# Kernel optimization log

Hardware: AMD Instinct MI355X
Metric: run time of the kernel (lower is better)

## Reference

```python
import jax, jax.numpy as jnp
import numpy as np

D_MODEL = 1024
H = 16
D_HEAD = D_MODEL // H


def setup_inputs() -> dict:
    key = jax.random.key(0)
    ks = jax.random.split(key, 9)
    B, S = 2, 2048
    x = jax.random.normal(ks[0], (B, S, D_MODEL), dtype=jnp.float32)
    s = 1.0 / np.sqrt(D_HEAD)
    # per-head Q/K/V linears, stacked: W[h, out, in], b[h, out] (torch Linear: y = x W^T + b)
    Wq = jax.random.normal(ks[1], (H, D_HEAD, D_HEAD), dtype=jnp.float32) * s
    bq = jax.random.normal(ks[2], (H, D_HEAD), dtype=jnp.float32) * 0.01
    Wk = jax.random.normal(ks[3], (H, D_HEAD, D_HEAD), dtype=jnp.float32) * s
    bk = jax.random.normal(ks[4], (H, D_HEAD), dtype=jnp.float32) * 0.01
    Wv = jax.random.normal(ks[5], (H, D_HEAD, D_HEAD), dtype=jnp.float32) * s
    bv = jax.random.normal(ks[6], (H, D_HEAD), dtype=jnp.float32) * 0.01
    Wo = jax.random.normal(ks[7], (D_MODEL, D_MODEL), dtype=jnp.float32) / np.sqrt(D_MODEL)
    bo = jax.random.normal(ks[8], (D_MODEL,), dtype=jnp.float32) * 0.01
    return {"x": x, "Wq": Wq, "bq": bq, "Wk": Wk, "bk": bk,
            "Wv": Wv, "bv": bv, "Wo": Wo, "bo": bo}


def reference(x, Wq, bq, Wk, bk, Wv, bv, Wo, bo):
    B, S, D = x.shape
    xh = x.reshape(B, S, H, D_HEAD)  # split along feature dim, head-major
    q = jnp.einsum('bshi,hoi->bsho', xh, Wq) + bq
    k = jnp.einsum('bshi,hoi->bsho', xh, Wk) + bk
    v = jnp.einsum('bshi,hoi->bsho', xh, Wv) + bv
    scale = 1.0 / jnp.sqrt(jnp.asarray(D_HEAD, dtype=x.dtype))  # source scales by sqrt(d_model//h)
    scores = jnp.einsum('bqhd,bkhd->bhqk', q, k) * scale
    causal = jnp.tril(jnp.ones((S, S), dtype=bool))
    scores = jnp.where(causal, scores, -jnp.inf)
    attn = jax.nn.softmax(scores, axis=-1)
    out = jnp.einsum('bhqk,bkhd->bqhd', attn, v).reshape(B, S, D)
    return out @ Wo.T + bo
```

## Files before the change

kernel.cpp:

```cpp
#include <hip/hip_runtime.h>
#include <cstddef>

#define Bc 2
#define Sc 2048
#define Dc 1024
#define Hc 16
#define QSC 0.18033688011112042f

typedef short short8 __attribute__((ext_vector_type(8)));
typedef float floatx4 __attribute__((ext_vector_type(4)));
typedef unsigned short ushort_t;

#if __has_builtin(__builtin_amdgcn_exp2f)
#define EXP2F(x) __builtin_amdgcn_exp2f(x)
#else
#define EXP2F(x) exp2f(x)
#endif

__device__ __forceinline__ unsigned pack2bf(float a, float b) {
    unsigned ua = __float_as_uint(a) + 0x8000u;
    unsigned ub = __float_as_uint(b) + 0x8000u;
    return __builtin_amdgcn_perm(ub, ua, 0x07060302u);
}
__device__ __forceinline__ ushort_t f2bf(float f) {
    return (ushort_t)((__float_as_uint(f) + 0x8000u) >> 16);
}

template<int N>
__device__ __forceinline__ float row_ror(float x) {
    return __int_as_float(__builtin_amdgcn_update_dpp(
        0, __float_as_int(x), 0x120 + N, 0xF, 0xF, false));
}
__device__ __forceinline__ float rsum16(float x) {
    x += row_ror<1>(x); x += row_ror<2>(x);
    x += row_ror<4>(x); x += row_ror<8>(x);
    return x;
}

__global__ __launch_bounds__(256) void wcvt_kernel(
    const float* __restrict__ Wo, const float* __restrict__ Wq,
    const float* __restrict__ Wk, const float* __restrict__ Wv,
    ushort_t* __restrict__ WoB, ushort_t* __restrict__ Wqkvb)
{
    int idx = (blockIdx.x * 256 + threadIdx.x) * 8;
    const float* src; ushort_t* dst;
    if (idx < 1048576) { src = Wo + idx; dst = WoB + idx; }
    else {
        int r = idx - 1048576;
        int w = r >> 16, off = r & 65535;
        src = (w == 0 ? Wq : (w == 1 ? Wk : Wv)) + off;
        dst = Wqkvb + r;
    }
    float4 a = *(const float4*)src;
    float4 c = *(const float4*)(src + 4);
    uint4 o;
    o.x = pack2bf(a.x, a.y); o.y = pack2bf(a.z, a.w);
    o.z = pack2bf(c.x, c.y); o.w = pack2bf(c.z, c.w);
    *(uint4*)dst = o;
}

__global__ __launch_bounds__(256) void qkv_kernel(
    const float* __restrict__ x, const ushort_t* __restrict__ Wqkvb,
    const float* __restrict__ bq, const float* __restrict__ bk, const float* __restrict__ bv,
    ushort_t* __restrict__ Qb, ushort_t* __restrict__ Kb, ushort_t* __restrict__ VT)
{
    const int blk = blockIdx.x;
    const int st = blk & 31, h = (blk >> 5) & 15, b = blk >> 9;
    const int bh = b * Hc + h, s0 = st * 64;
    const int tid = threadIdx.x, wid = tid >> 6, lane = tid & 63;
    const int lr = lane & 15, quad = lane >> 4;

    __shared__ ushort_t Xs[64 * 72];
    __shared__ ushort_t Wsh[3 * 64 * 72];

    {
        int row = tid >> 2, cg = tid & 3;
        const float* xp = x + ((size_t)(b * Sc + s0 + row)) * Dc + h * 64 + cg * 16;
        float4 v0 = *(const float4*)xp;
        float4 v1 = *(const float4*)(xp + 4);
        float4 v2 = *(const float4*)(xp + 8);
        float4 v3 = *(const float4*)(xp + 12);
        uint4 p0, p1;
        p0.x = pack2bf(v0.x, v0.y); p0.y = pack2bf(v0.z, v0.w);
        p0.z = pack2bf(v1.x, v1.y); p0.w = pack2bf(v1.z, v1.w);
        p1.x = pack2bf(v2.x, v2.y); p1.y = pack2bf(v2.z, v2.w);
        p1.z = pack2bf(v3.x, v3.y); p1.w = pack2bf(v3.z, v3.w);
        *(uint4*)(Xs + row * 72 + cg * 16) = p0;
        *(uint4*)(Xs + row * 72 + cg * 16 + 8) = p1;
    }
    {
        const ushort_t* Wg = Wqkvb + (size_t)h * 4096;
#pragma unroll
        for (int s = 0; s < 6; ++s) {
            int c = tid + s * 256;
            int w = c >> 9, rem = c & 511, row = rem >> 3, part = rem & 7;
            *(short8*)(Wsh + (w * 64 + row) * 72 + part * 8) =
                *(const short8*)(Wg + (size_t)w * 65536 + row * 64 + part * 8);
        }
    }
    __syncthreads();

    short8 af0 = *(const short8*)(Xs + (wid * 16 + lr) * 72 + quad * 8);
    short8 af1 = *(const short8*)(Xs + (wid * 16 + lr) * 72 + 32 + quad * 8);

    const float* bias3[3] = {bq + h * 64, bk + h * 64, bv + h * 64};
    const int row = tid >> 2, cg = tid & 3;

#pragma unroll
    for (int w = 0; w < 3; ++w) {
        ushort_t* Ot = Wsh + w * 64 * 72;
        short8 bf0[4], bf1[4];
#pragma unroll
        for (int n = 0; n < 4; ++n) {
            const ushort_t* wrow = Ot + (n * 16 + lr) * 72;
            bf0[n] = *(const short8*)(wrow + quad * 8);
            bf1[n] = *(const short8*)(wrow + 32 + quad * 8);
        }
        floatx4 acc[4];
#pragma unroll
        for (int n = 0; n < 4; ++n) {
            floatx4 z = {0.f, 0.f, 0.f, 0.f};
            acc[n] = __builtin_amdgcn_mfma_f32_16x16x32_bf16(af0, bf0[n], z, 0, 0, 0);
            acc[n] = __builtin_amdgcn_mfma_f32_16x16x32_bf16(af1, bf1[n], acc[n], 0, 0, 0);
        }
        __syncthreads();
        if (w < 2) {
#pragma unroll
            for (int n = 0; n < 4; ++n) {
                float bias = bias3[w][n * 16 + lr];
#pragma unroll
                for (int r = 0; r < 4; ++r) {
                    float val = acc[n][r] + bias;
                    if (w == 0) val *= QSC;
                    Ot[(wid * 16 + quad * 4 + r) * 72 + n * 16 + lr] = f2bf(val);
                }
            }
        } else {
#pragma unroll
            for (int n = 0; n < 4; ++n) {
                float bias = bias3[2][n * 16 + lr];
                uint2 pw;
                pw.x = pack2bf(acc[n][0] + bias, acc[n][1] + bias);
                pw.y = pack2bf(acc[n][2] + bias, acc[n][3] + bias);
                *(uint2*)(Ot + (n * 16 + lr) * 72 + wid * 16 + quad * 4) = pw;
            }
        }
        __syncthreads();
        const ushort_t* srcp = Ot + row * 72 + cg * 16;
        uint4 d0 = *(const uint4*)srcp;
        uint4 d1 = *(const uint4*)(srcp + 8);
        ushort_t* dst;
        if (w == 0)      dst = Qb + ((size_t)bh * Sc + s0 + row) * 64 + cg * 16;
        else if (w == 1) dst = Kb + ((size_t)bh * Sc + s0 + row) * 64 + cg * 16;
        else             dst = VT + ((size_t)bh * 64 + row) * Sc + s0 + cg * 16;
        *(uint4*)dst = d0;
        *(uint4*)(dst + 8) = d1;
    }
}

#define ST 72

__global__ __launch_bounds__(128) void attn_kernel(
    const ushort_t* __restrict__ Qg, const ushort_t* __restrict__ Kg,
    const ushort_t* __restrict__ VTg, ushort_t* __restrict__ Actx)
{
    const int blk = blockIdx.x;
    const int u = blk & 255;
    const int bh = u & 31;
    const int f = (u >> 5) & 7;
    const int tpair = (blk < 256) ? f : 15 - f;
    const int b = bh >> 4, h = bh & 15;
    const int qta = 31 - tpair, qtb = tpair;
    const int s0a = qta * 64, s0b = qtb * 64;
    const int tid = threadIdx.x, wid = tid >> 6, lane = tid & 63;
    const int lr = lane & 15, quad = lane >> 4;

    __shared__ ushort_t Ks[64 * ST];
    __shared__ ushort_t Vs[64 * ST];
    __shared__ ushort_t Ps[8 * 16 * ST];

    const ushort_t* Kbh = Kg + (size_t)bh * Sc * 64;
    const ushort_t* Vbh = VTg + (size_t)bh * 64 * Sc;

    short8 qa[2][2], qb[2][2];
#pragma unroll
    for (int g = 0; g < 2; ++g) {
        const ushort_t* QrA = Qg + ((size_t)bh * Sc + s0a + wid * 32 + g * 16 + lr) * 64;
        const ushort_t* QrB = Qg + ((size_t)bh * Sc + s0b + wid * 32 + g * 16 + lr) * 64;
        qa[g][0] = *(const short8*)(QrA + quad * 8);
        qa[g][1] = *(const short8*)(QrA + 32 + quad * 8);
        qb[g][0] = *(const short8*)(QrB + quad * 8);
        qb[g][1] = *(const short8*)(QrB + 32 + quad * 8);
    }

    floatx4 oA[2][4], oB[2][4];
    float lA[2][4], lB[2][4];
#pragma unroll
    for (int g = 0; g < 2; ++g)
#pragma unroll
        for (int n = 0; n < 4; ++n) { oA[g][n] = floatx4{0,0,0,0}; oB[g][n] = floatx4{0,0,0,0}; }
#pragma unroll
    for (int g = 0; g < 2; ++g)
#pragma unroll
        for (int r = 0; r < 4; ++r) { lA[g][r] = 0.f; lB[g][r] = 0.f; }

    const int sr = tid >> 3, sp = tid & 7;

    short8 kr[4], vr[4];
#pragma unroll
    for (int s = 0; s < 4; ++s) {
        kr[s] = *(const short8*)(Kbh + (size_t)(sr + s * 16) * 64 + sp * 8);
        vr[s] = *(const short8*)(Vbh + (size_t)(sr + s * 16) * Sc + sp * 8);
    }
#pragma unroll
    for (int s = 0; s < 4; ++s) {
        *(short8*)(Ks + (sr + s * 16) * ST + sp * 8) = kr[s];
        *(short8*)(Vs + (sr + s * 16) * ST + sp * 8) = vr[s];
    }
    __syncthreads();

    for (int kt = 0; kt <= qta; ++kt) {
        const bool hasB = (kt <= qtb);

        short8 kf[4][2];
#pragma unroll
        for (int kg = 0; kg < 4; ++kg) {
            const ushort_t* kp = Ks + (4 * lr + kg) * ST;
            kf[kg][0] = *(const short8*)(kp + quad * 8);
            kf[kg][1] = *(const short8*)(kp + 32 + quad * 8);
        }

        if (kt < qta) {
            const ushort_t* kn = Kbh + (size_t)(kt + 1) * 4096;
            const ushort_t* vn = Vbh + (kt + 1) * 64;
#pragma unroll
            for (int s = 0; s < 4; ++s) {
                kr[s] = *(const short8*)(kn + (size_t)(sr + s * 16) * 64 + sp * 8);
                vr[s] = *(const short8*)(vn + (size_t)(sr + s * 16) * Sc + sp * 8);
            }
        }

#pragma unroll
        for (int g = 0; g < 2; ++g) {
            floatx4 s4[4];
#pragma unroll
            for (int kg = 0; kg < 4; ++kg) {
                floatx4 z = {0.f, 0.f, 0.f, 0.f};
                floatx4 t0 = __builtin_amdgcn_mfma_f32_16x16x32_bf16(qa[g][0], kf[kg][0], z, 0, 0, 0);
                s4[kg] = __builtin_amdgcn_mfma_f32_16x16x32_bf16(qa[g][1], kf[kg][1], t0, 0, 0, 0);
            }
            if (kt == qta) {
#pragma unroll
                for (int kg = 0; kg < 4; ++kg) {
                    int key = 4 * lr + kg;
#pragma unroll
                    for (int r = 0; r < 4; ++r)
                        if (key > wid * 32 + g * 16 + quad * 4 + r) s4[kg][r] = -1e30f;
                }
            }
            ushort_t* Pg = Ps + ((wid * 2 + g) * 16) * ST;
#pragma unroll
            for (int r = 0; r < 4; ++r) {
                float p0 = EXP2F(s4[0][r]), p1 = EXP2F(s4[1][r]);
                float p2 = EXP2F(s4[2][r]), p3 = EXP2F(s4[3][r]);
                lA[g][r] += rsum16(p0 + p1 + p2 + p3);
                uint2 pw; pw.x = pack2bf(p0, p1); pw.y = pack2bf(p2, p3);
                *(uint2*)(Pg + (quad * 4 + r) * ST + 4 * lr) = pw;
            }
        }
        if (hasB) {
#pragma unroll
            for (int g = 0; g < 2; ++g) {
                floatx4 s4[4];
#pragma unroll
                for (int kg = 0; kg < 4; ++kg) {
                    floatx4 z = {0.f, 0.f, 0.f, 0.f};
                    floatx4 t0 = __builtin_amdgcn_mfma_f32_16x16x32_bf16(qb[g][0], kf[kg][0], z, 0, 0, 0);
                    s4[kg] = __builtin_amdgcn_mfma_f32_16x16x32_bf16(qb[g][1], kf[kg][1], t0, 0, 0, 0);
                }
                if (kt == qtb) {
#pragma unroll
                    for (int kg = 0; kg < 4; ++kg) {
                        int key = 4 * lr + kg;
#pragma unroll
                        for (int r = 0; r < 4; ++r)
                            if (key > wid * 32 + g * 16 + quad * 4 + r) s4[kg][r] = -1e30f;
                    }
                }
                ushort_t* Pg = Ps + (((2 + wid) * 2 + g) * 16) * ST;
#pragma unroll
                for (int r = 0; r < 4; ++r) {
                    float p0 = EXP2F(s4[0][r]), p1 = EXP2F(s4[1][r]);
                    float p2 = EXP2F(s4[2][r]), p3 = EXP2F(s4[3][r]);
                    lB[g][r] += rsum16(p0 + p1 + p2 + p3);
                    uint2 pw; pw.x = pack2bf(p0, p1); pw.y = pack2bf(p2, p3);
                    *(uint2*)(Pg + (quad * 4 + r) * ST + 4 * lr) = pw;
                }
            }
        }

        short8 vf[4][2];
#pragma unroll
        for (int n = 0; n < 4; ++n) {
            const ushort_t* vp = Vs + (n * 16 + lr) * ST;
            vf[n][0] = *(const short8*)(vp + quad * 8);
            vf[n][1] = *(const short8*)(vp + 32 + quad * 8);
        }

#pragma unroll
        for (int g = 0; g < 2; ++g) {
            const ushort_t* Pg = Ps + ((wid * 2 + g) * 16) * ST;
            short8 pf0 = *(const short8*)(Pg + lr * ST + quad * 8);
            short8 pf1 = *(const short8*)(Pg + lr * ST + 32 + quad * 8);
#pragma unroll
            for (int n = 0; n < 4; ++n) {
                oA[g][n] = __builtin_amdgcn_mfma_f32_16x16x32_bf16(pf0, vf[n][0], oA[g][n], 0, 0, 0);
                oA[g][n] = __builtin_amdgcn_mfma_f32_16x16x32_bf16(pf1, vf[n][1], oA[g][n], 0, 0, 0);
            }
        }
        if (hasB) {
#pragma unroll
            for (int g = 0; g < 2; ++g) {
                const ushort_t* Pg = Ps + (((2 + wid) * 2 + g) * 16) * ST;
                short8 pf0 = *(const short8*)(Pg + lr * ST + quad * 8);
                short8 pf1 = *(const short8*)(Pg + lr * ST + 32 + quad * 8);
#pragma unroll
                for (int n = 0; n < 4; ++n) {
                    oB[g][n] = __builtin_amdgcn_mfma_f32_16x16x32_bf16(pf0, vf[n][0], oB[g][n], 0, 0, 0);
                    oB[g][n] = __builtin_amdgcn_mfma_f32_16x16x32_bf16(pf1, vf[n][1], oB[g][n], 0, 0, 0);
                }
            }
        }

        __syncthreads();
        if (kt < qta) {
#pragma unroll
            for (int s = 0; s < 4; ++s) {
                *(short8*)(Ks + (sr + s * 16) * ST + sp * 8) = kr[s];
                *(short8*)(Vs + (sr + s * 16) * ST + sp * 8) = vr[s];
            }
            __syncthreads();
        }
    }

#pragma unroll
    for (int g = 0; g < 2; ++g) {
#pragma unroll
        for (int r = 0; r < 4; ++r) {
            float invA = 1.f / lA[g][r], invB = 1.f / lB[g][r];
            int rowA = s0a + wid * 32 + g * 16 + quad * 4 + r;
            int rowB = s0b + wid * 32 + g * 16 + quad * 4 + r;
            ushort_t* dA = Actx + ((size_t)(b * Sc + rowA)) * Dc + h * 64 + lr;
            ushort_t* dB = Actx + ((size_t)(b * Sc + rowB)) * Dc + h * 64 + lr;
#pragma unroll
            for (int n = 0; n < 4; ++n) {
                dA[n * 16] = f2bf(oA[g][n][r] * invA);
                dB[n * 16] = f2bf(oB[g][n][r] * invB);
            }
        }
    }
}

__global__ __launch_bounds__(256, 2) void proj_kernel(
    const ushort_t* __restrict__ Ab, const ushort_t* __restrict__ Wb,
    const float* __restrict__ bo, float* __restrict__ out)
{
    const int bn = blockIdx.x & 15, bm = blockIdx.x >> 4;
    const int tid = threadIdx.x, wid = tid >> 6, lane = tid & 63;
    const int lr = lane & 15, quad = lane >> 4;
    const int wm = wid * 32;

    __shared__ ushort_t As[128 * 40];
    __shared__ ushort_t Bs[64 * 40];

    floatx4 acc[2][4];
#pragma unroll
    for (int i = 0; i < 2; ++i)
#pragma unroll
        for (int n = 0; n < 4; ++n) acc[i][n] = floatx4{0.f, 0.f, 0.f, 0.f};

    const ushort_t* Ag = Ab + (size_t)bm * 128 * 1024;
    const ushort_t* Wg = Wb + (size_t)bn * 64 * 1024;

    const int ar0 = tid >> 2, ap0 = tid & 3;
    const int ar1 = ar0 + 64;

    short8 a0 = *(const short8*)(Ag + (size_t)ar0 * 1024 + ap0 * 8);
    short8 a1 = *(const short8*)(Ag + (size_t)ar1 * 1024 + ap0 * 8);
    short8 b0 = *(const short8*)(Wg + (size_t)ar0 * 1024 + ap0 * 8);
    *(short8*)(As + ar0 * 40 + ap0 * 8) = a0;
    *(short8*)(As + ar1 * 40 + ap0 * 8) = a1;
    *(short8*)(Bs + ar0 * 40 + ap0 * 8) = b0;
    __syncthreads();

    for (int k0 = 0; k0 < 1024; k0 += 32) {
        short8 fa0 = *(const short8*)(As + (wm + lr) * 40 + quad * 8);
        short8 fa1 = *(const short8*)(As + (wm + 16 + lr) * 40 + quad * 8);
        short8 fb[4];
#pragma unroll
        for (int n = 0; n < 4; ++n)
            fb[n] = *(const short8*)(Bs + (n * 16 + lr) * 40 + quad * 8);

        if (k0 < 992) {
            int k1 = k0 + 32;
            a0 = *(const short8*)(Ag + (size_t)ar0 * 1024 + k1 + ap0 * 8);
            a1 = *(const short8*)(Ag + (size_t)ar1 * 1024 + k1 + ap0 * 8);
            b0 = *(const short8*)(Wg + (size_t)ar0 * 1024 + k1 + ap0 * 8);
        }
#pragma unroll
        for (int n = 0; n < 4; ++n) {
            acc[0][n] = __builtin_amdgcn_mfma_f32_16x16x32_bf16(fa0, fb[n], acc[0][n], 0, 0, 0);
            acc[1][n] = __builtin_amdgcn_mfma_f32_16x16x32_bf16(fa1, fb[n], acc[1][n], 0, 0, 0);
        }
        __syncthreads();
        if (k0 < 992) {
            *(short8*)(As + ar0 * 40 + ap0 * 8) = a0;
            *(short8*)(As + ar1 * 40 + ap0 * 8) = a1;
            *(short8*)(Bs + ar0 * 40 + ap0 * 8) = b0;
            __syncthreads();
        }
    }

#pragma unroll
    for (int i = 0; i < 2; ++i) {
        int mrow = bm * 128 + wm + i * 16 + quad * 4;
#pragma unroll
        for (int n = 0; n < 4; ++n) {
            int col = bn * 64 + n * 16 + lr;
            float bias = bo[col];
#pragma unroll
            for (int r = 0; r < 4; ++r)
                out[(size_t)(mrow + r) * 1024 + col] = acc[i][n][r] + bias;
        }
    }
}

extern "C" void kernel_launch(void* const* d_in, const int* in_sizes, int n_in,
                              void* d_out, int out_size, void* d_ws, size_t ws_size,
                              hipStream_t stream)
{
    (void)in_sizes; (void)n_in; (void)out_size; (void)ws_size;
    const float* x  = (const float*)d_in[0];
    const float* Wq = (const float*)d_in[1];
    const float* bq = (const float*)d_in[2];
    const float* Wk = (const float*)d_in[3];
    const float* bk = (const float*)d_in[4];
    const float* Wv = (const float*)d_in[5];
    const float* bv = (const float*)d_in[6];
    const float* Wo = (const float*)d_in[7];
    const float* bo = (const float*)d_in[8];
    float* out = (float*)d_out;

    const size_t N4 = (size_t)Bc * Hc * Sc * 64;
    ushort_t* base  = (ushort_t*)d_ws;
    ushort_t* Qb    = base;
    ushort_t* Kb    = base + N4;
    ushort_t* VT    = base + 2 * N4;
    ushort_t* Actx  = base + 3 * N4;
    ushort_t* WoB   = base + 4 * N4;
    ushort_t* Wqkvb = base + 4 * N4 + 1048576;

    wcvt_kernel<<<dim3(608), dim3(256), 0, stream>>>(Wo, Wq, Wk, Wv, WoB, Wqkvb);
    qkv_kernel<<<dim3(Bc * Hc * (Sc / 64)), dim3(256), 0, stream>>>(
        x, Wqkvb, bq, bk, bv, Qb, Kb, VT);
    attn_kernel<<<dim3(512), dim3(128), 0, stream>>>(Qb, Kb, VT, Actx);
    proj_kernel<<<dim3(32 * 16), dim3(256), 0, stream>>>(Actx, WoB, bo, out);
}
```

Measured before the change: 170.2 us.

## Split attention key range across two blocks and combine with normalization kernel

Each paired query-tile attention block is split into two halves over the key range, doubling the grid from 512 to 1024 blocks so the 256 CUs get more work and load balance improves. Each half writes unnormalized fp32 partial outputs and row sums to workspace, and a new kernel adds the two partials, normalizes, and converts to bf16 for the projection. This works without max-rescaling because the softmax skips max subtraction. The cost is extra fp32 global traffic, one more kernel launch, and duplicated Q loads.

```diff
diff --git a/kernel.cpp b/kernel.cpp
--- a/kernel.cpp
+++ b/kernel.cpp
@@ -162,55 +162,63 @@
 
 __global__ __launch_bounds__(128) void attn_kernel(
     const ushort_t* __restrict__ Qg, const ushort_t* __restrict__ Kg,
-    const ushort_t* __restrict__ VTg, ushort_t* __restrict__ Actx)
+    const ushort_t* __restrict__ VTg,
+    float* __restrict__ Of0, float* __restrict__ Of1,
+    float* __restrict__ Lf0, float* __restrict__ Lf1)
 {
     const int blk = blockIdx.x;
-    const int u = blk & 255;
-    const int bh = u & 31;
-    const int f = (u >> 5) & 7;
-    const int tpair = (blk < 256) ? f : 15 - f;
+    const int bh = blk & 31;
+    const int g5 = blk >> 5;
+    const int half = g5 & 1;
+    const int q = g5 >> 1;
+    const int qta = 31 - q, qtb = q;
+    const int mid = (qta + 2) >> 1;
+    const int kt0 = half ? mid : 0;
+    const int ktE = half ? qta : mid - 1;
+    const int s0a = qta * 64, s0b = qtb * 64;
     const int b = bh >> 4, h = bh & 15;
-    const int qta = 31 - tpair, qtb = tpair;
-    const int s0a = qta * 64, s0b = qtb * 64;
     const int tid = threadIdx.x, wid = tid >> 6, lane = tid & 63;
     const int lr = lane & 15, quad = lane >> 4;
 
     __shared__ ushort_t Ks[64 * ST];
     __shared__ ushort_t Vs[64 * ST];
-    __shared__ ushort_t Ps[8 * 16 * ST];
+    __shared__ __align__(16) ushort_t Ps[8 * 16 * ST];
+
+    float* Of = half ? Of1 : Of0;
+    float* Lf = half ? Lf1 : Lf0;
 
     const ushort_t* Kbh = Kg + (size_t)bh * Sc * 64;
     const ushort_t* Vbh = VTg + (size_t)bh * 64 * Sc;
 
     short8 qa[2][2], qb[2][2];
 #pragma unroll
-    for (int g = 0; g < 2; ++g) {
-        const ushort_t* QrA = Qg + ((size_t)bh * Sc + s0a + wid * 32 + g * 16 + lr) * 64;
-        const ushort_t* QrB = Qg + ((size_t)bh * Sc + s0b + wid * 32 + g * 16 + lr) * 64;
-        qa[g][0] = *(const short8*)(QrA + quad * 8);
-        qa[g][1] = *(const short8*)(QrA + 32 + quad * 8);
-        qb[g][0] = *(const short8*)(QrB + quad * 8);
-        qb[g][1] = *(const short8*)(QrB + 32 + quad * 8);
+    for (int gg = 0; gg < 2; ++gg) {
+        const ushort_t* QrA = Qg + ((size_t)bh * Sc + s0a + wid * 32 + gg * 16 + lr) * 64;
+        const ushort_t* QrB = Qg + ((size_t)bh * Sc + s0b + wid * 32 + gg * 16 + lr) * 64;
+        qa[gg][0] = *(const short8*)(QrA + quad * 8);
+        qa[gg][1] = *(const short8*)(QrA + 32 + quad * 8);
+        qb[gg][0] = *(const short8*)(QrB + quad * 8);
+        qb[gg][1] = *(const short8*)(QrB + 32 + quad * 8);
     }
 
     floatx4 oA[2][4], oB[2][4];
     float lA[2][4], lB[2][4];
 #pragma unroll
-    for (int g = 0; g < 2; ++g)
-#pragma unroll
-        for (int n = 0; n < 4; ++n) { oA[g][n] = floatx4{0,0,0,0}; oB[g][n] = floatx4{0,0,0,0}; }
-#pragma unroll
-    for (int g = 0; g < 2; ++g)
-#pragma unroll
-        for (int r = 0; r < 4; ++r) { lA[g][r] = 0.f; lB[g][r] = 0.f; }
+    for (int gg = 0; gg < 2; ++gg)
+#pragma unroll
+        for (int n = 0; n < 4; ++n) { oA[gg][n] = floatx4{0,0,0,0}; oB[gg][n] = floatx4{0,0,0,0}; }
+#pragma unroll
+    for (int gg = 0; gg < 2; ++gg)
+#pragma unroll
+        for (int r = 0; r < 4; ++r) { lA[gg][r] = 0.f; lB[gg][r] = 0.f; }
 
     const int sr = tid >> 3, sp = tid & 7;
 
     short8 kr[4], vr[4];
 #pragma unroll
     for (int s = 0; s < 4; ++s) {
-        kr[s] = *(const short8*)(Kbh + (size_t)(sr + s * 16) * 64 + sp * 8);
-        vr[s] = *(const short8*)(Vbh + (size_t)(sr + s * 16) * Sc + sp * 8);
+        kr[s] = *(const short8*)(Kbh + ((size_t)kt0 * 64 + sr + s * 16) * 64 + sp * 8);
+        vr[s] = *(const short8*)(Vbh + (size_t)(sr + s * 16) * Sc + kt0 * 64 + sp * 8);
     }
 #pragma unroll
     for (int s = 0; s < 4; ++s) {
@@ -219,7 +227,7 @@
     }
     __syncthreads();
 
-    for (int kt = 0; kt <= qta; ++kt) {
+    for (int kt = kt0; kt <= ktE; ++kt) {
         const bool hasB = (kt <= qtb);
 
         short8 kf[4][2];
@@ -230,7 +238,7 @@
             kf[kg][1] = *(const short8*)(kp + 32 + quad * 8);
         }
 
-        if (kt < qta) {
+        if (kt < ktE) {
             const ushort_t* kn = Kbh + (size_t)(kt + 1) * 4096;
             const ushort_t* vn = Vbh + (kt + 1) * 64;
 #pragma unroll
@@ -241,13 +249,13 @@
         }
 
 #pragma unroll
-        for (int g = 0; g < 2; ++g) {
+        for (int gg = 0; gg < 2; ++gg) {
             floatx4 s4[4];
 #pragma unroll
             for (int kg = 0; kg < 4; ++kg) {
                 floatx4 z = {0.f, 0.f, 0.f, 0.f};
-                floatx4 t0 = __builtin_amdgcn_mfma_f32_16x16x32_bf16(qa[g][0], kf[kg][0], z, 0, 0, 0);
-                s4[kg] = __builtin_amdgcn_mfma_f32_16x16x32_bf16(qa[g][1], kf[kg][1], t0, 0, 0, 0);
+                floatx4 t0 = __builtin_amdgcn_mfma_f32_16x16x32_bf16(qa[gg][0], kf[kg][0], z, 0, 0, 0);
+                s4[kg] = __builtin_amdgcn_mfma_f32_16x16x32_bf16(qa[gg][1], kf[kg][1], t0, 0, 0, 0);
             }
             if (kt == qta) {
 #pragma unroll
@@ -255,28 +263,28 @@
                     int key = 4 * lr + kg;
 #pragma unroll
                     for (int r = 0; r < 4; ++r)
-                        if (key > wid * 32 + g * 16 + quad * 4 + r) s4[kg][r] = -1e30f;
+                        if (key > wid * 32 + gg * 16 + quad * 4 + r) s4[kg][r] = -1e30f;
                 }
             }
-            ushort_t* Pg = Ps + ((wid * 2 + g) * 16) * ST;
+            ushort_t* Pg = Ps + ((wid * 2 + gg) * 16) * ST;
 #pragma unroll
             for (int r = 0; r < 4; ++r) {
                 float p0 = EXP2F(s4[0][r]), p1 = EXP2F(s4[1][r]);
                 float p2 = EXP2F(s4[2][r]), p3 = EXP2F(s4[3][r]);
-                lA[g][r] += rsum16(p0 + p1 + p2 + p3);
+                lA[gg][r] += rsum16(p0 + p1 + p2 + p3);
                 uint2 pw; pw.x = pack2bf(p0, p1); pw.y = pack2bf(p2, p3);
                 *(uint2*)(Pg + (quad * 4 + r) * ST + 4 * lr) = pw;
             }
         }
         if (hasB) {
 #pragma unroll
-            for (int g = 0; g < 2; ++g) {
+            for (int gg = 0; gg < 2; ++gg) {
                 floatx4 s4[4];
 #pragma unroll
                 for (int kg = 0; kg < 4; ++kg) {
                     floatx4 z = {0.f, 0.f, 0.f, 0.f};
-                    floatx4 t0 = __builtin_amdgcn_mfma_f32_16x16x32_bf16(qb[g][0], kf[kg][0], z, 0, 0, 0);
-                    s4[kg] = __builtin_amdgcn_mfma_f32_16x16x32_bf16(qb[g][1], kf[kg][1], t0, 0, 0, 0);
+                    floatx4 t0 = __builtin_amdgcn_mfma_f32_16x16x32_bf16(qb[gg][0], kf[kg][0], z, 0, 0, 0);
+                    s4[kg] = __builtin_amdgcn_mfma_f32_16x16x32_bf16(qb[gg][1], kf[kg][1], t0, 0, 0, 0);
                 }
                 if (kt == qtb) {
 #pragma unroll
@@ -284,15 +292,15 @@
                         int key = 4 * lr + kg;
 #pragma unroll
                         for (int r = 0; r < 4; ++r)
-                            if (key > wid * 32 + g * 16 + quad * 4 + r) s4[kg][r] = -1e30f;
+                            if (key > wid * 32 + gg * 16 + quad * 4 + r) s4[kg][r] = -1e30f;
                     }
                 }
-                ushort_t* Pg = Ps + (((2 + wid) * 2 + g) * 16) * ST;
+                ushort_t* Pg = Ps + (((2 + wid) * 2 + gg) * 16) * ST;
 #pragma unroll
                 for (int r = 0; r < 4; ++r) {
                     float p0 = EXP2F(s4[0][r]), p1 = EXP2F(s4[1][r]);
                     float p2 = EXP2F(s4[2][r]), p3 = EXP2F(s4[3][r]);
-                    lB[g][r] += rsum16(p0 + p1 + p2 + p3);
+                    lB[gg][r] += rsum16(p0 + p1 + p2 + p3);
                     uint2 pw; pw.x = pack2bf(p0, p1); pw.y = pack2bf(p2, p3);
                     *(uint2*)(Pg + (quad * 4 + r) * ST + 4 * lr) = pw;
                 }
@@ -308,32 +316,32 @@
         }
 
 #pragma unroll
-        for (int g = 0; g < 2; ++g) {
-            const ushort_t* Pg = Ps + ((wid * 2 + g) * 16) * ST;
+        for (int gg = 0; gg < 2; ++gg) {
+            const ushort_t* Pg = Ps + ((wid * 2 + gg) * 16) * ST;
             short8 pf0 = *(const short8*)(Pg + lr * ST + quad * 8);
             short8 pf1 = *(const short8*)(Pg + lr * ST + 32 + quad * 8);
 #pragma unroll
             for (int n = 0; n < 4; ++n) {
-                oA[g][n] = __builtin_amdgcn_mfma_f32_16x16x32_bf16(pf0, vf[n][0], oA[g][n], 0, 0, 0);
-                oA[g][n] = __builtin_amdgcn_mfma_f32_16x16x32_bf16(pf1, vf[n][1], oA[g][n], 0, 0, 0);
+                oA[gg][n] = __builtin_amdgcn_mfma_f32_16x16x32_bf16(pf0, vf[n][0], oA[gg][n], 0, 0, 0);
+                oA[gg][n] = __builtin_amdgcn_mfma_f32_16x16x32_bf16(pf1, vf[n][1], oA[gg][n], 0, 0, 0);
             }
         }
         if (hasB) {
 #pragma unroll
-            for (int g = 0; g < 2; ++g) {
-                const ushort_t* Pg = Ps + (((2 + wid) * 2 + g) * 16) * ST;
+            for (int gg = 0; gg < 2; ++gg) {
+                const ushort_t* Pg = Ps + (((2 + wid) * 2 + gg) * 16) * ST;
                 short8 pf0 = *(const short8*)(Pg + lr * ST + quad * 8);
                 short8 pf1 = *(const short8*)(Pg + lr * ST + 32 + quad * 8);
 #pragma unroll
                 for (int n = 0; n < 4; ++n) {
-                    oB[g][n] = __builtin_amdgcn_mfma_f32_16x16x32_bf16(pf0, vf[n][0], oB[g][n], 0, 0, 0);
-                    oB[g][n] = __builtin_amdgcn_mfma_f32_16x16x32_bf16(pf1, vf[n][1], oB[g][n], 0, 0, 0);
+                    oB[gg][n] = __builtin_amdgcn_mfma_f32_16x16x32_bf16(pf0, vf[n][0], oB[gg][n], 0, 0, 0);
+                    oB[gg][n] = __builtin_amdgcn_mfma_f32_16x16x32_bf16(pf1, vf[n][1], oB[gg][n], 0, 0, 0);
                 }
             }
         }
 
         __syncthreads();
-        if (kt < qta) {
+        if (kt < ktE) {
 #pragma unroll
             for (int s = 0; s < 4; ++s) {
                 *(short8*)(Ks + (sr + s * 16) * ST + sp * 8) = kr[s];
@@ -343,22 +351,72 @@
         }
     }
 
-#pragma unroll
-    for (int g = 0; g < 2; ++g) {
-#pragma unroll
-        for (int r = 0; r < 4; ++r) {
-            float invA = 1.f / lA[g][r], invB = 1.f / lB[g][r];
-            int rowA = s0a + wid * 32 + g * 16 + quad * 4 + r;
-            int rowB = s0b + wid * 32 + g * 16 + quad * 4 + r;
-            ushort_t* dA = Actx + ((size_t)(b * Sc + rowA)) * Dc + h * 64 + lr;
-            ushort_t* dB = Actx + ((size_t)(b * Sc + rowB)) * Dc + h * 64 + lr;
-#pragma unroll
-            for (int n = 0; n < 4; ++n) {
-                dA[n * 16] = f2bf(oA[g][n][r] * invA);
-                dB[n * 16] = f2bf(oB[g][n][r] * invB);
-            }
-        }
-    }
+    if (lr == 0) {
+#pragma unroll
+        for (int gg = 0; gg < 2; ++gg)
+#pragma unroll
+            for (int r = 0; r < 4; ++r) {
+                int rw = wid * 32 + gg * 16 + quad * 4 + r;
+                Lf[(size_t)bh * Sc + s0a + rw] = lA[gg][r];
+                Lf[(size_t)bh * Sc + s0b + rw] = lB[gg][r];
+            }
+    }
+
+    float* Osw = (float*)Ps;
+    const int orow = tid >> 1, ohalf = (tid & 1) * 32;
+#pragma unroll
+    for (int t = 0; t < 2; ++t) {
+#pragma unroll
+        for (int gg = 0; gg < 2; ++gg)
+#pragma unroll
+            for (int n = 0; n < 4; ++n)
+#pragma unroll
+                for (int r = 0; r < 4; ++r)
+                    Osw[(wid * 32 + gg * 16 + quad * 4 + r) * 68 + n * 16 + lr] =
+                        (t == 0) ? oA[gg][n][r] : oB[gg][n][r];
+        __syncthreads();
+        const float* srcp = Osw + orow * 68 + ohalf;
+        float* dstp = Of + ((size_t)bh * Sc + (t == 0 ? s0a : s0b) + orow) * 64 + ohalf;
+#pragma unroll
+        for (int i = 0; i < 8; ++i)
+            *(float4*)(dstp + 4 * i) = *(const float4*)(srcp + 4 * i);
+        __syncthreads();
+    }
+}
+
+__global__ __launch_bounds__(256) void nrm_kernel(
+    const float* __restrict__ Of0, const float* __restrict__ Of1,
+    const float* __restrict__ Lf0, const float* __restrict__ Lf1,
+    ushort_t* __restrict__ Actx)
+{
+    int idx = blockIdx.x * 256 + threadIdx.x;
+    int row = idx >> 2;
+    int seg = idx & 3;
+    int bh = row >> 11, s = row & 2047;
+    int b = bh >> 4, h = bh & 15;
+    float inv = 1.f / (Lf0[row] + Lf1[row]);
+    const float* p0 = Of0 + (size_t)row * 64 + seg * 16;
+    const float* p1 = Of1 + (size_t)row * 64 + seg * 16;
+    ushort_t* dst = Actx + ((size_t)(b * Sc + s)) * Dc + h * 64 + seg * 16;
+    uint4 o0, o1;
+    {
+        float4 a0 = *(const float4*)p0,       b0 = *(const float4*)p1;
+        float4 a1 = *(const float4*)(p0 + 4), b1 = *(const float4*)(p1 + 4);
+        o0.x = pack2bf((a0.x + b0.x) * inv, (a0.y + b0.y) * inv);
+        o0.y = pack2bf((a0.z + b0.z) * inv, (a0.w + b0.w) * inv);
+        o0.z = pack2bf((a1.x + b1.x) * inv, (a1.y + b1.y) * inv);
+        o0.w = pack2bf((a1.z + b1.z) * inv, (a1.w + b1.w) * inv);
+    }
+    {
+        float4 a0 = *(const float4*)(p0 + 8),  b0 = *(const float4*)(p1 + 8);
+        float4 a1 = *(const float4*)(p0 + 12), b1 = *(const float4*)(p1 + 12);
+        o1.x = pack2bf((a0.x + b0.x) * inv, (a0.y + b0.y) * inv);
+        o1.y = pack2bf((a0.z + b0.z) * inv, (a0.w + b0.w) * inv);
+        o1.z = pack2bf((a1.x + b1.x) * inv, (a1.y + b1.y) * inv);
+        o1.w = pack2bf((a1.z + b1.z) * inv, (a1.w + b1.w) * inv);
+    }
+    *(uint4*)dst = o0;
+    *(uint4*)(dst + 8) = o1;
 }
 
 __global__ __launch_bounds__(256, 2) void proj_kernel(
@@ -459,10 +517,16 @@
     ushort_t* Actx  = base + 3 * N4;
     ushort_t* WoB   = base + 4 * N4;
     ushort_t* Wqkvb = base + 4 * N4 + 1048576;
+    float* fbase = (float*)(base + 4 * N4 + 1048576 + 196608);
+    float* Of0 = fbase;
+    float* Of1 = fbase + N4;
+    float* Lf0 = fbase + 2 * N4;
+    float* Lf1 = fbase + 2 * N4 + 65536;
 
     wcvt_kernel<<<dim3(608), dim3(256), 0, stream>>>(Wo, Wq, Wk, Wv, WoB, Wqkvb);
     qkv_kernel<<<dim3(Bc * Hc * (Sc / 64)), dim3(256), 0, stream>>>(
         x, Wqkvb, bq, bk, bv, Qb, Kb, VT);
-    attn_kernel<<<dim3(512), dim3(128), 0, stream>>>(Qb, Kb, VT, Actx);
+    attn_kernel<<<dim3(1024), dim3(128), 0, stream>>>(Qb, Kb, VT, Of0, Of1, Lf0, Lf1);
+    nrm_kernel<<<dim3(1024), dim3(256), 0, stream>>>(Of0, Of1, Lf0, Lf1, Actx);
     proj_kernel<<<dim3(32 * 16), dim3(256), 0, stream>>>(Actx, WoB, bo, out);
 }
```

Result: slower. 176.3 us (+3.6%).
